# Performance work log

Hardware: AMD Instinct MI355X
Metric: run time of the kernel (lower is better)

The kernel has to match this reference:

```python
import jax, jax.numpy as jnp
import numpy as np

VOCAB, EMB, HID = 32000, 128, 128
B, S = 8, 1024


def setup_inputs() -> dict:
    key = jax.random.key(0)
    ks = jax.random.split(key, 8)
    scale_e = 1.0  # nn.Embedding default N(0,1)
    k_rnn = 1.0 / np.sqrt(HID)  # nn.RNN uniform(-1/sqrt(H), 1/sqrt(H))
    k_fc = 1.0 / np.sqrt(HID)
    return {
        "x": jax.random.randint(ks[0], (B, S), 0, VOCAB),
        "emb_table": jax.random.normal(ks[1], (VOCAB, EMB), dtype=jnp.float32) * scale_e,
        "W_ih": jax.random.uniform(ks[2], (HID, EMB), jnp.float32, -k_rnn, k_rnn),
        "b_ih": jax.random.uniform(ks[3], (HID,), jnp.float32, -k_rnn, k_rnn),
        "W_hh": jax.random.uniform(ks[4], (HID, HID), jnp.float32, -k_rnn, k_rnn),
        "b_hh": jax.random.uniform(ks[5], (HID,), jnp.float32, -k_rnn, k_rnn),
        "fc_W": jax.random.uniform(ks[6], (VOCAB, HID), jnp.float32, -k_fc, k_fc),
        "fc_b": jax.random.uniform(ks[7], (VOCAB,), jnp.float32, -k_fc, k_fc),
    }


def reference(x, emb_table, W_ih, b_ih, W_hh, b_hh, fc_W, fc_b):
    # Embedding lookup: [B,S,E]
    e = emb_table[x]
    # Precompute input projection for all timesteps: [B,S,H]
    x_proj = jnp.einsum("bse,he->bsh", e, W_ih) + b_ih + b_hh

    h0 = jnp.zeros((x.shape[0], W_hh.shape[0]), dtype=e.dtype)

    def step(h, xp_t):  # xp_t: [B,H]
        h_new = jnp.tanh(xp_t + h @ W_hh.T)
        return h_new, h_new

    # scan over time: xs [S,B,H]
    h_last, hs = jax.lax.scan(step, h0, jnp.swapaxes(x_proj, 0, 1))
    outputs = jnp.swapaxes(hs, 0, 1)  # [B,S,H]
    logits = jnp.einsum("bsh,vh->bsv", outputs, fc_W) + fc_b  # [B,S,V]
    hidden_state = h_last[None]  # [1,B,H] matching torch num_layers dim
    return logits, hidden_state
```

## Files before the change

kernel.cpp:

```cpp
#include <hip/hip_runtime.h>
#include <hip/hip_bf16.h>

#define VOCAB 32000
#define EMB   128
#define HID   128
#define BB    8
#define SS    1024

typedef __bf16 bf16x8_t __attribute__((ext_vector_type(8)));
typedef float  f32x4_t  __attribute__((ext_vector_type(4)));

__device__ __forceinline__ float dpp_xor1(float x) {
    return __int_as_float(__builtin_amdgcn_update_dpp(
        0, __float_as_int(x), 0xB1, 0xF, 0xF, true));
}
__device__ __forceinline__ float dpp_xor2(float x) {
    return __int_as_float(__builtin_amdgcn_update_dpp(
        0, __float_as_int(x), 0x4E, 0xF, 0xF, true));
}

__global__ __launch_bounds__(512) void xproj_kernel(
    const int* __restrict__ x, const float* __restrict__ emb,
    const float* __restrict__ W_ih, const float* __restrict__ b_ih,
    const float* __restrict__ b_hh, float* __restrict__ xp)
{
    const int t  = threadIdx.x;
    const int h  = t >> 2;
    const int ks = t & 3;

    float w[32];
    {
        const float* wr = W_ih + h * EMB + ks * 32;
        #pragma unroll
        for (int i = 0; i < 32; i += 4) {
            float4 v = *(const float4*)(wr + i);
            w[i] = v.x; w[i+1] = v.y; w[i+2] = v.z; w[i+3] = v.w;
        }
    }
    const float bias = b_ih[h] + b_hh[h];

    __shared__ float el[2][EMB];
    const int base = blockIdx.x * 32;

    float4 v = make_float4(0.f, 0.f, 0.f, 0.f);
    if (t < 32) v = *(const float4*)(emb + (size_t)x[base] * EMB + t * 4);

    for (int r = 0; r < 32; ++r) {
        if (t < 32) *(float4*)(&el[r & 1][t * 4]) = v;
        __syncthreads();
        if (t < 32 && r + 1 < 32)
            v = *(const float4*)(emb + (size_t)x[base + r + 1] * EMB + t * 4);

        float a0 = 0.f, a1 = 0.f, a2 = 0.f, a3 = 0.f;
        const float* e = &el[r & 1][ks * 32];
        #pragma unroll
        for (int c = 0; c < 8; ++c) {
            float4 hv = *(const float4*)(e + c * 4);
            a0 = fmaf(w[c*4+0], hv.x, a0);
            a1 = fmaf(w[c*4+1], hv.y, a1);
            a2 = fmaf(w[c*4+2], hv.z, a2);
            a3 = fmaf(w[c*4+3], hv.w, a3);
        }
        float sum = (a0 + a1) + (a2 + a3);
        sum += __shfl_xor(sum, 1);
        sum += __shfl_xor(sum, 2);
        if (ks == 0) xp[(size_t)(base + r) * HID + h] = bias + sum;
    }
}

__global__ __launch_bounds__(256) void convert_bf16_kernel(
    const float* __restrict__ in, __hip_bfloat16* __restrict__ out)
{
    const size_t i = ((size_t)blockIdx.x * 256 + threadIdx.x) * 8;
    float4 a = *(const float4*)(in + i);
    float4 b = *(const float4*)(in + i + 4);
    union { __hip_bfloat16 h[8]; uint4 u; } p;
    p.h[0] = __float2bfloat16(a.x); p.h[1] = __float2bfloat16(a.y);
    p.h[2] = __float2bfloat16(a.z); p.h[3] = __float2bfloat16(a.w);
    p.h[4] = __float2bfloat16(b.x); p.h[5] = __float2bfloat16(b.y);
    p.h[6] = __float2bfloat16(b.z); p.h[7] = __float2bfloat16(b.w);
    *(uint4*)(out + i) = p.u;
}

__global__ __launch_bounds__(256) void mega_kernel(
    const float* __restrict__ xp, const float* __restrict__ W_hh,
    __hip_bfloat16* __restrict__ hs_bf16, float* __restrict__ hidden_out,
    const __hip_bfloat16* __restrict__ Wb, const float* __restrict__ fc_b,
    float* __restrict__ C, unsigned int* __restrict__ prog)
{
    const int bid = blockIdx.x;

    if (bid < BB) {
        const int b  = bid;
        const int t  = threadIdx.x;
        const int w  = t >> 6;
        const int l  = t & 63;
        const int ks = l & 3;
        const int g  = l >> 2;
        const int jb = w * 16 + g;

        f32x4_t wr[2][8];
        #pragma unroll
        for (int m = 0; m < 2; ++m) {
            const float* src = W_hh + (size_t)(jb + 64 * m) * HID + ks * 32;
            #pragma unroll
            for (int i = 0; i < 8; ++i) wr[m][i] = *(const f32x4_t*)(src + i * 4);
        }

        __shared__ float hbuf[2][160];
        if (t < 160) hbuf[0][t] = 0.f;

        const float* xpb = xp + (size_t)b * SS * HID;
        const bool  wrt  = (ks == 0);
        const int rbase = ks * 40;

        float xsA[8][2], xsB[8][2];
        if (wrt) {
            #pragma unroll
            for (int u = 0; u < 8; ++u) {
                xsA[u][0] = xpb[(size_t)u * HID + jb];
                xsA[u][1] = xpb[(size_t)u * HID + jb + 64];
            }
        }
        __syncthreads();

#define RNN_SUPERSTEP(XC, XN, BASE)                                          \
    {                                                                        \
        const int nbase_ = (BASE) + 8;                                       \
        if (wrt && nbase_ < SS) {                                            \
            _Pragma("unroll")                                                \
            for (int u = 0; u < 8; ++u) {                                    \
                XN[u][0] = xpb[(size_t)(nbase_ + u) * HID + jb];             \
                XN[u][1] = xpb[(size_t)(nbase_ + u) * HID + jb + 64];        \
            }                                                                \
        }                                                                    \
        _Pragma("unroll")                                                    \
        for (int u = 0; u < 8; ++u) {                                        \
            const int step_ = (BASE) + u;                                    \
            const float* hc_ = hbuf[u & 1];                                  \
            f32x4_t hv[8];                                                   \
            _Pragma("unroll")                                                \
            for (int i = 0; i < 4; ++i)                                      \
                hv[i] = *(const f32x4_t*)(hc_ + rbase + i * 4);              \
            _Pragma("unroll")                                                \
            for (int i = 4; i < 8; ++i)                                      \
                hv[i] = *(const f32x4_t*)(hc_ + rbase + 4 + i * 4);          \
            f32x4_t a0 = {0.f,0.f,0.f,0.f}, a1 = a0, c0 = a0, c1 = a0;       \
            _Pragma("unroll")                                                \
            for (int i = 0; i < 4; ++i) {                                    \
                a0 += wr[0][i]   * hv[i];                                    \
                a1 += wr[0][i+4] * hv[i+4];                                  \
                c0 += wr[1][i]   * hv[i];                                    \
                c1 += wr[1][i+4] * hv[i+4];                                  \
            }                                                                \
            f32x4_t av = a0 + a1, cv = c0 + c1;                              \
            float s0 = (av.x + av.y) + (av.z + av.w);                        \
            float s1 = (cv.x + cv.y) + (cv.z + cv.w);                        \
            s0 += dpp_xor1(s0);  s0 += dpp_xor2(s0);                         \
            s1 += dpp_xor1(s1);  s1 += dpp_xor2(s1);                         \
            if (wrt) {                                                       \
                const float z0 = XC[u][0] + s0;                              \
                const float e0 = __expf(2.0f * z0);                          \
                const float h0 = 1.0f - 2.0f * __builtin_amdgcn_rcpf(e0 + 1.0f); \
                const float z1 = XC[u][1] + s1;                              \
                const float e1 = __expf(2.0f * z1);                          \
                const float h1 = 1.0f - 2.0f * __builtin_amdgcn_rcpf(e1 + 1.0f); \
                const int j0 = jb, j1 = jb + 64;                             \
                hbuf[(u + 1) & 1][j0 + ((j0 >> 4) << 2)] = h0;               \
                hbuf[(u + 1) & 1][j1 + ((j1 >> 4) << 2)] = h1;               \
                hs_bf16[((size_t)b * SS + step_) * HID + j0] = __float2bfloat16(h0); \
                hs_bf16[((size_t)b * SS + step_) * HID + j1] = __float2bfloat16(h1); \
                if (step_ == SS - 1) {                                       \
                    hidden_out[b * HID + j0] = h0;                           \
                    hidden_out[b * HID + j1] = h1;                           \
                }                                                            \
            }                                                                \
            asm volatile("s_waitcnt lgkmcnt(0)" ::: "memory");               \
            __builtin_amdgcn_s_barrier();                                    \
        }                                                                    \
    }

        for (int chunk = 0; chunk < 8; ++chunk) {
            for (int sb2 = 0; sb2 < 8; ++sb2) {
                const int base = chunk * 128 + sb2 * 16;
                RNN_SUPERSTEP(xsA, xsB, base);
                RNN_SUPERSTEP(xsB, xsA, base + 8);
            }
            asm volatile("s_waitcnt vmcnt(0)" ::: "memory");
            __builtin_amdgcn_s_barrier();
            if (t == 0)
                __hip_atomic_store(&prog[b], (unsigned)(chunk + 1),
                                   __ATOMIC_RELEASE, __HIP_MEMORY_SCOPE_AGENT);
        }
#undef RNN_SUPERSTEP
    } else {
        const int cid  = bid - BB;
        const int NC   = 256 - BB;
        const int t    = threadIdx.x;
        const int lane = t & 63;
        const int cw   = t >> 6;
        const int wm   = cw >> 1;
        const int wn   = cw & 1;
        const int lr   = lane & 15;
        const int kq   = lane >> 4;

        for (int tc = 0; tc < 8; ++tc) {
            if (t == 0) {
                for (int b2 = 0; b2 < BB; ++b2) {
                    while (__hip_atomic_fetch_add(&prog[b2], 0u,
                               __ATOMIC_RELAXED, __HIP_MEMORY_SCOPE_AGENT)
                           < (unsigned)(tc + 1))
                        __builtin_amdgcn_s_sleep(32);
                }
            }
            __syncthreads();
            __builtin_amdgcn_fence(__ATOMIC_ACQUIRE, "agent");

            for (int i = cid; i < 2000; i += NC) {
                const int b2 = i / 250;
                const int nb = i % 250;
                const int mb = b2 * 8 + tc;
                const int m0 = mb * 128 + wm * 64;
                const int n0 = nb * 128 + wn * 64;

                const __hip_bfloat16* Arow = hs_bf16 + (size_t)(m0 + lr) * HID + kq * 8;
                const __hip_bfloat16* Wrow = Wb      + (size_t)(n0 + lr) * HID + kq * 8;

                f32x4_t acc[4][4];
                #pragma unroll
                for (int ii = 0; ii < 4; ++ii)
                    #pragma unroll
                    for (int jj = 0; jj < 4; ++jj)
                        acc[ii][jj] = (f32x4_t){0.f, 0.f, 0.f, 0.f};

                bf16x8_t af[2][4], bw[2][4];
                #pragma unroll
                for (int mt = 0; mt < 4; ++mt)
                    af[0][mt] = *(const bf16x8_t*)(Arow + mt * 16 * HID);
                #pragma unroll
                for (int nt = 0; nt < 4; ++nt)
                    bw[0][nt] = *(const bf16x8_t*)(Wrow + nt * 16 * HID);

                #pragma unroll
                for (int kk = 0; kk < 4; ++kk) {
                    const int cur = kk & 1, nxt = cur ^ 1;
                    if (kk < 3) {
                        const int off = (kk + 1) * 32;
                        #pragma unroll
                        for (int mt = 0; mt < 4; ++mt)
                            af[nxt][mt] = *(const bf16x8_t*)(Arow + mt * 16 * HID + off);
                        #pragma unroll
                        for (int nt = 0; nt < 4; ++nt)
                            bw[nxt][nt] = *(const bf16x8_t*)(Wrow + nt * 16 * HID + off);
                    }
                    #pragma unroll
                    for (int mt = 0; mt < 4; ++mt)
                        #pragma unroll
                        for (int nt = 0; nt < 4; ++nt)
                            acc[mt][nt] = __builtin_amdgcn_mfma_f32_16x16x32_bf16(
                                bw[cur][nt], af[cur][mt], acc[mt][nt], 0, 0, 0);
                }

                const int vq = kq * 4;
                #pragma unroll
                for (int nt = 0; nt < 4; ++nt) {
                    const int v0 = n0 + nt * 16 + vq;
                    float4 fb = *(const float4*)(fc_b + v0);
                    const f32x4_t fbv = {fb.x, fb.y, fb.z, fb.w};
                    #pragma unroll
                    for (int mt = 0; mt < 4; ++mt) {
                        const int row = m0 + mt * 16 + lr;
                        *(f32x4_t*)(C + (size_t)row * VOCAB + v0) = acc[mt][nt] + fbv;
                    }
                }
            }
        }
    }
}

extern "C" void kernel_launch(void* const* d_in, const int* in_sizes, int n_in,
                              void* d_out, int out_size, void* d_ws, size_t ws_size,
                              hipStream_t stream)
{
    const int*   x    = (const int*)  d_in[0];
    const float* emb  = (const float*)d_in[1];
    const float* W_ih = (const float*)d_in[2];
    const float* b_ih = (const float*)d_in[3];
    const float* W_hh = (const float*)d_in[4];
    const float* b_hh = (const float*)d_in[5];
    const float* fc_W = (const float*)d_in[6];
    const float* fc_b = (const float*)d_in[7];

    float* logits = (float*)d_out;
    float* hidden = logits + (size_t)BB * SS * VOCAB;

    char* ws = (char*)d_ws;
    float*           xpb = (float*)ws;
    __hip_bfloat16*  hsb = (__hip_bfloat16*)(ws + 4194304);
    __hip_bfloat16*  fwb = (__hip_bfloat16*)(ws + 6291456);
    unsigned int*    prg = (unsigned int*)(ws + 14483456);

    hipMemsetAsync(prg, 0, 64, stream);
    xproj_kernel<<<dim3(256), dim3(512), 0, stream>>>(x, emb, W_ih, b_ih, b_hh, xpb);
    convert_bf16_kernel<<<dim3(2000), dim3(256), 0, stream>>>(fc_W, fwb);
    mega_kernel<<<dim3(256), dim3(256), 0, stream>>>(xpb, W_hh, hsb, hidden,
                                                     fwb, fc_b, logits, prg);
}
```

Before: 556.7 us.

## Split tanh finalization across lanes and consume RNN chunks per batch as ready

In the recurrent blocks, lanes ks==0 and ks==1 now each finalize one hidden unit (tanh, LDS write, bf16 store) instead of one lane doing two. This halves the serial tail per step on the critical path. The GEMM consumer blocks now wait on each batch's progress counter separately and process that batch's tiles immediately, rather than waiting for all 8 batches first. The poll sleep is also shortened, trading more syncthreads and polling traffic for earlier overlap with the recurrence.

```diff
diff --git a/kernel.cpp b/kernel.cpp
--- a/kernel.cpp
+++ b/kernel.cpp
@@ -98,6 +98,7 @@
         const int ks = l & 3;
         const int g  = l >> 2;
         const int jb = w * 16 + g;
+        const int jw = jb + 64 * ks;
 
         f32x4_t wr[2][8];
         #pragma unroll
@@ -111,28 +112,25 @@
         if (t < 160) hbuf[0][t] = 0.f;
 
         const float* xpb = xp + (size_t)b * SS * HID;
-        const bool  wrt  = (ks == 0);
+        const bool  fin  = (ks < 2);
         const int rbase = ks * 40;
-
-        float xsA[8][2], xsB[8][2];
-        if (wrt) {
+        const int wword = jw + ((jw >> 4) << 2);
+
+        float xsA[8], xsB[8];
+        if (fin) {
             #pragma unroll
-            for (int u = 0; u < 8; ++u) {
-                xsA[u][0] = xpb[(size_t)u * HID + jb];
-                xsA[u][1] = xpb[(size_t)u * HID + jb + 64];
-            }
+            for (int u = 0; u < 8; ++u)
+                xsA[u] = xpb[(size_t)u * HID + jw];
         }
         __syncthreads();
 
 #define RNN_SUPERSTEP(XC, XN, BASE)                                          \
     {                                                                        \
         const int nbase_ = (BASE) + 8;                                       \
-        if (wrt && nbase_ < SS) {                                            \
-            _Pragma("unroll")                                                \
-            for (int u = 0; u < 8; ++u) {                                    \
-                XN[u][0] = xpb[(size_t)(nbase_ + u) * HID + jb];             \
-                XN[u][1] = xpb[(size_t)(nbase_ + u) * HID + jb + 64];        \
-            }                                                                \
+        if (fin && nbase_ < SS) {                                            \
+            _Pragma("unroll")                                                \
+            for (int u = 0; u < 8; ++u)                                      \
+                XN[u] = xpb[(size_t)(nbase_ + u) * HID + jw];                \
         }                                                                    \
         _Pragma("unroll")                                                    \
         for (int u = 0; u < 8; ++u) {                                        \
@@ -158,22 +156,14 @@
             float s1 = (cv.x + cv.y) + (cv.z + cv.w);                        \
             s0 += dpp_xor1(s0);  s0 += dpp_xor2(s0);                         \
             s1 += dpp_xor1(s1);  s1 += dpp_xor2(s1);                         \
-            if (wrt) {                                                       \
-                const float z0 = XC[u][0] + s0;                              \
-                const float e0 = __expf(2.0f * z0);                          \
-                const float h0 = 1.0f - 2.0f * __builtin_amdgcn_rcpf(e0 + 1.0f); \
-                const float z1 = XC[u][1] + s1;                              \
-                const float e1 = __expf(2.0f * z1);                          \
-                const float h1 = 1.0f - 2.0f * __builtin_amdgcn_rcpf(e1 + 1.0f); \
-                const int j0 = jb, j1 = jb + 64;                             \
-                hbuf[(u + 1) & 1][j0 + ((j0 >> 4) << 2)] = h0;               \
-                hbuf[(u + 1) & 1][j1 + ((j1 >> 4) << 2)] = h1;               \
-                hs_bf16[((size_t)b * SS + step_) * HID + j0] = __float2bfloat16(h0); \
-                hs_bf16[((size_t)b * SS + step_) * HID + j1] = __float2bfloat16(h1); \
-                if (step_ == SS - 1) {                                       \
-                    hidden_out[b * HID + j0] = h0;                           \
-                    hidden_out[b * HID + j1] = h1;                           \
-                }                                                            \
+            if (fin) {                                                       \
+                const float sm = (ks == 0) ? s0 : s1;                        \
+                const float z  = XC[u] + sm;                                 \
+                const float e  = __expf(2.0f * z);                           \
+                const float hn = 1.0f - 2.0f * __builtin_amdgcn_rcpf(e + 1.0f); \
+                hbuf[(u + 1) & 1][wword] = hn;                               \
+                hs_bf16[((size_t)b * SS + step_) * HID + jw] = __float2bfloat16(hn); \
+                if (step_ == SS - 1) hidden_out[b * HID + jw] = hn;          \
             }                                                                \
             asm volatile("s_waitcnt lgkmcnt(0)" ::: "memory");               \
             __builtin_amdgcn_s_barrier();                                    \
@@ -205,72 +195,71 @@
         const int kq   = lane >> 4;
 
         for (int tc = 0; tc < 8; ++tc) {
-            if (t == 0) {
-                for (int b2 = 0; b2 < BB; ++b2) {
+            for (int b2 = 0; b2 < BB; ++b2) {
+                if (t == 0) {
                     while (__hip_atomic_fetch_add(&prog[b2], 0u,
                                __ATOMIC_RELAXED, __HIP_MEMORY_SCOPE_AGENT)
                            < (unsigned)(tc + 1))
-                        __builtin_amdgcn_s_sleep(32);
+                        __builtin_amdgcn_s_sleep(16);
                 }
-            }
-            __syncthreads();
-            __builtin_amdgcn_fence(__ATOMIC_ACQUIRE, "agent");
-
-            for (int i = cid; i < 2000; i += NC) {
-                const int b2 = i / 250;
-                const int nb = i % 250;
+                __syncthreads();
+                __builtin_amdgcn_fence(__ATOMIC_ACQUIRE, "agent");
+
                 const int mb = b2 * 8 + tc;
                 const int m0 = mb * 128 + wm * 64;
-                const int n0 = nb * 128 + wn * 64;
-
-                const __hip_bfloat16* Arow = hs_bf16 + (size_t)(m0 + lr) * HID + kq * 8;
-                const __hip_bfloat16* Wrow = Wb      + (size_t)(n0 + lr) * HID + kq * 8;
-
-                f32x4_t acc[4][4];
-                #pragma unroll
-                for (int ii = 0; ii < 4; ++ii)
-                    #pragma unroll
-                    for (int jj = 0; jj < 4; ++jj)
-                        acc[ii][jj] = (f32x4_t){0.f, 0.f, 0.f, 0.f};
-
-                bf16x8_t af[2][4], bw[2][4];
-                #pragma unroll
-                for (int mt = 0; mt < 4; ++mt)
-                    af[0][mt] = *(const bf16x8_t*)(Arow + mt * 16 * HID);
-                #pragma unroll
-                for (int nt = 0; nt < 4; ++nt)
-                    bw[0][nt] = *(const bf16x8_t*)(Wrow + nt * 16 * HID);
-
-                #pragma unroll
-                for (int kk = 0; kk < 4; ++kk) {
-                    const int cur = kk & 1, nxt = cur ^ 1;
-                    if (kk < 3) {
-                        const int off = (kk + 1) * 32;
+
+                for (int nb = cid; nb < 250; nb += NC) {
+                    const int n0 = nb * 128 + wn * 64;
+
+                    const __hip_bfloat16* Arow = hs_bf16 + (size_t)(m0 + lr) * HID + kq * 8;
+                    const __hip_bfloat16* Wrow = Wb      + (size_t)(n0 + lr) * HID + kq * 8;
+
+                    f32x4_t acc[4][4];
+                    #pragma unroll
+                    for (int ii = 0; ii < 4; ++ii)
+                        #pragma unroll
+                        for (int jj = 0; jj < 4; ++jj)
+                            acc[ii][jj] = (f32x4_t){0.f, 0.f, 0.f, 0.f};
+
+                    bf16x8_t af[2][4], bw[2][4];
+                    #pragma unroll
+                    for (int mt = 0; mt < 4; ++mt)
+                        af[0][mt] = *(const bf16x8_t*)(Arow + mt * 16 * HID);
+                    #pragma unroll
+                    for (int nt = 0; nt < 4; ++nt)
+                        bw[0][nt] = *(const bf16x8_t*)(Wrow + nt * 16 * HID);
+
+                    #pragma unroll
+                    for (int kk = 0; kk < 4; ++kk) {
+                        const int cur = kk & 1, nxt = cur ^ 1;
+                        if (kk < 3) {
+                            const int off = (kk + 1) * 32;
+                            #pragma unroll
+                            for (int mt = 0; mt < 4; ++mt)
+                                af[nxt][mt] = *(const bf16x8_t*)(Arow + mt * 16 * HID + off);
+                            #pragma unroll
+                            for (int nt = 0; nt < 4; ++nt)
+                                bw[nxt][nt] = *(const bf16x8_t*)(Wrow + nt * 16 * HID + off);
+                        }
                         #pragma unroll
                         for (int mt = 0; mt < 4; ++mt)
-                            af[nxt][mt] = *(const bf16x8_t*)(Arow + mt * 16 * HID + off);
+                            #pragma unroll
+                            for (int nt = 0; nt < 4; ++nt)
+                                acc[mt][nt] = __builtin_amdgcn_mfma_f32_16x16x32_bf16(
+                                    bw[cur][nt], af[cur][mt], acc[mt][nt], 0, 0, 0);
+                    }
+
+                    const int vq = kq * 4;
+                    #pragma unroll
+                    for (int nt = 0; nt < 4; ++nt) {
+                        const int v0 = n0 + nt * 16 + vq;
+                        float4 fb = *(const float4*)(fc_b + v0);
+                        const f32x4_t fbv = {fb.x, fb.y, fb.z, fb.w};
                         #pragma unroll
-                        for (int nt = 0; nt < 4; ++nt)
-                            bw[nxt][nt] = *(const bf16x8_t*)(Wrow + nt * 16 * HID + off);
-                    }
-                    #pragma unroll
-                    for (int mt = 0; mt < 4; ++mt)
-                        #pragma unroll
-                        for (int nt = 0; nt < 4; ++nt)
-                            acc[mt][nt] = __builtin_amdgcn_mfma_f32_16x16x32_bf16(
-                                bw[cur][nt], af[cur][mt], acc[mt][nt], 0, 0, 0);
-                }
-
-                const int vq = kq * 4;
-                #pragma unroll
-                for (int nt = 0; nt < 4; ++nt) {
-                    const int v0 = n0 + nt * 16 + vq;
-                    float4 fb = *(const float4*)(fc_b + v0);
-                    const f32x4_t fbv = {fb.x, fb.y, fb.z, fb.w};
-                    #pragma unroll
-                    for (int mt = 0; mt < 4; ++mt) {
-                        const int row = m0 + mt * 16 + lr;
-                        *(f32x4_t*)(C + (size_t)row * VOCAB + v0) = acc[mt][nt] + fbv;
+                        for (int mt = 0; mt < 4; ++mt) {
+                            const int row = m0 + mt * 16 + lr;
+                            *(f32x4_t*)(C + (size_t)row * VOCAB + v0) = acc[mt][nt] + fbv;
+                        }
                     }
                 }
             }
```

Measured after the change: 965.8 us. 1.73x slower.
